# Performance work log

Measured on AMD Instinct MI355X. Metric: run time of the kernel, lower is better.

Reference implementation:

```python
import jax, jax.numpy as jnp
import numpy as np

HIDDEN = 1024
N_HEADS = 16
HEAD_DIM = HIDDEN // N_HEADS
WINDOW = 256
HALF_W = WINDOW // 2  # 128
GLOBAL_TOKENS = (0,)


def setup_inputs() -> dict:
    key = jax.random.key(0)
    ks = jax.random.split(key, 5)
    B, S = 1, 4096
    scale = 0.02
    return {
        "x": jax.random.normal(ks[0], (B, S, HIDDEN), dtype=jnp.float32),
        "Wq": jax.random.normal(ks[1], (HIDDEN, HIDDEN), dtype=jnp.float32) * scale,
        "Wk": jax.random.normal(ks[2], (HIDDEN, HIDDEN), dtype=jnp.float32) * scale,
        "Wv": jax.random.normal(ks[3], (HIDDEN, HIDDEN), dtype=jnp.float32) * scale,
        "Wo": jax.random.normal(ks[4], (HIDDEN, HIDDEN), dtype=jnp.float32) * scale,
    }


def _longformer_mask(seq_len: int) -> jnp.ndarray:
    # sliding window |i-j| <= half_w, plus full rows/cols for global tokens
    idx = jnp.arange(seq_len)
    mask = jnp.abs(idx[:, None] - idx[None, :]) <= HALF_W
    for g in GLOBAL_TOKENS:
        if 0 <= g < seq_len:
            mask = mask.at[g, :].set(True)
            mask = mask.at[:, g].set(True)
    return mask  # [S, S] bool


def reference(x, Wq, Wk, Wv, Wo):
    B, S, H = x.shape
    scale = HEAD_DIM ** -0.5
    # nn.Linear(bias=False): y = x @ W.T ; split heads -> [B, nH, S, hd]
    def proj(W):
        return jnp.einsum('bsh,oh->bso', x, W).reshape(B, S, N_HEADS, HEAD_DIM).transpose(0, 2, 1, 3)
    q, k, v = proj(Wq), proj(Wk), proj(Wv)
    scores = jnp.einsum('bnsd,bntd->bnst', q, k) * scale  # [B, nH, S, S]
    mask = _longformer_mask(S)
    scores = jnp.where(mask[None, None], scores, jnp.float32(-jnp.inf))
    attn = jax.nn.softmax(scores, axis=-1)
    out = jnp.einsum('bnst,bntd->bnsd', attn, v)  # [B, nH, S, hd]
    out = out.transpose(0, 2, 1, 3).reshape(B, S, H)
    return jnp.einsum('bsh,oh->bso', out, Wo)
```

## Files before the change

### kernel.cpp

```cpp
#include <hip/hip_runtime.h>
#include <hip/hip_bf16.h>
#include <stdint.h>

#define S_LEN 4096
#define HID   1024
#define NH    16
#define HD    64
#define HWIN  128

typedef __bf16 bf16x8 __attribute__((ext_vector_type(8)));
typedef float  f32x4  __attribute__((ext_vector_type(4)));
typedef unsigned short u16x8 __attribute__((ext_vector_type(8)));

typedef const __attribute__((address_space(1))) unsigned int* gas_ptr;
typedef __attribute__((address_space(3))) unsigned int* las_ptr;

__device__ __forceinline__ float bf2f(unsigned short u) {
  union { float f; uint32_t i; } w; w.i = ((uint32_t)u) << 16; return w.f;
}
__device__ __forceinline__ unsigned short f2bf(float f) {
  union { float f; uint32_t i; } w; w.f = f;
  uint32_t r = (w.i + 0x7FFFu + ((w.i >> 16) & 1u)) >> 16;
  return (unsigned short)r;
}

__device__ __forceinline__ void gld_lds16(const void* g, void* l) {
  __builtin_amdgcn_global_load_lds((gas_ptr)g, (las_ptr)l, 16, 0, 0);
}

__global__ __launch_bounds__(256) void convert_all(
    const float* __restrict__ x,
    const float* __restrict__ wq, const float* __restrict__ wk,
    const float* __restrict__ wv, const float* __restrict__ wo,
    unsigned short* __restrict__ xb,
    unsigned short* __restrict__ wqb, unsigned short* __restrict__ wkb,
    unsigned short* __restrict__ wvb, unsigned short* __restrict__ wob) {
  const int XF4 = (S_LEN * HID) / 4;
  const int WF4 = (HID * HID) / 4;
  int i = blockIdx.x * 256 + threadIdx.x;
#pragma unroll
  for (int it = 0; it < 4; it++, i += 524288) {
    const float* in; unsigned short* out; int off;
    if (i < XF4) { in = x; out = xb; off = i; }
    else {
      int j = i - XF4;
      int w = j >> 18;
      off = j & (WF4 - 1);
      switch (w) {
        case 0:  in = wq; out = wqb; break;
        case 1:  in = wk; out = wkb; break;
        case 2:  in = wv; out = wvb; break;
        default: in = wo; out = wob; break;
      }
    }
    float4 v = reinterpret_cast<const float4*>(in)[off];
    ushort4 o;
    o.x = f2bf(v.x); o.y = f2bf(v.y); o.z = f2bf(v.z); o.w = f2bf(v.w);
    reinterpret_cast<ushort4*>(out)[off] = o;
  }
}

__device__ __forceinline__ void gemm_body(const unsigned short* __restrict__ A,
                                          const unsigned short* __restrict__ B,
                                          unsigned short* __restrict__ Cb, int mode) {
  __shared__ __align__(16) unsigned short SM[2 * 128 * 64];
  unsigned short* As = SM;
  unsigned short* Bs = SM + 128 * 64;
  constexpr int K = HID;
  const int tid  = threadIdx.x;
  const int lane = tid & 63;
  const int wave = tid >> 6;
  const int wm = wave >> 1, wn = wave & 1;
  const int m0 = blockIdx.x * 128;
  const int n0 = blockIdx.y * 128;
  const int cl = lane & 15, g = lane >> 4;

  f32x4 acc[4][4];
#pragma unroll
  for (int i = 0; i < 4; i++)
#pragma unroll
    for (int j = 0; j < 4; j++) acc[i][j] = f32x4{0.f, 0.f, 0.f, 0.f};

  const unsigned short* Ap[4];
  const unsigned short* Bp[4];
  int ldso[4];
#pragma unroll
  for (int u = 0; u < 4; u++) {
    int s = tid + u * 256;
    int row = s >> 3, c16 = s & 7;
    int sc = ((c16 ^ (row & 7)) << 3);
    Ap[u] = A + (size_t)(m0 + row) * K + sc;
    Bp[u] = B + (size_t)(n0 + row) * K + sc;
    ldso[u] = s * 8;
  }

  for (int k0 = 0; k0 < K; k0 += 64) {
#pragma unroll
    for (int u = 0; u < 4; u++) {
      gld_lds16(Ap[u] + k0, &As[ldso[u]]);
      gld_lds16(Bp[u] + k0, &Bs[ldso[u]]);
    }
    __syncthreads();
#pragma unroll
    for (int kk = 0; kk < 2; kk++) {
      bf16x8 a[4], b[4];
#pragma unroll
      for (int mi = 0; mi < 4; mi++) {
        int row = wm * 64 + mi * 16 + cl;
        int c16 = (kk * 4 + g) ^ (row & 7);
        a[mi] = *reinterpret_cast<const bf16x8*>(&As[row * 64 + c16 * 8]);
      }
#pragma unroll
      for (int ni = 0; ni < 4; ni++) {
        int row = wn * 64 + ni * 16 + cl;
        int c16 = (kk * 4 + g) ^ (row & 7);
        b[ni] = *reinterpret_cast<const bf16x8*>(&Bs[row * 64 + c16 * 8]);
      }
#pragma unroll
      for (int mi = 0; mi < 4; mi++)
#pragma unroll
        for (int ni = 0; ni < 4; ni++)
          acc[mi][ni] = __builtin_amdgcn_mfma_f32_16x16x32_bf16(a[mi], b[ni], acc[mi][ni], 0, 0, 0);
    }
    __syncthreads();
  }

  const int rl = g * 4;
  if (mode == 1) {
#pragma unroll
    for (int mi = 0; mi < 4; mi++)
#pragma unroll
      for (int ni = 0; ni < 4; ni++) {
        int c = wn * 64 + ni * 16 + cl;
        int slot = (wm * 16 + mi * 4 + g) ^ ((c & 7) << 2);
        uint2 u;
        u.x = (uint32_t)f2bf(acc[mi][ni][0]) | ((uint32_t)f2bf(acc[mi][ni][1]) << 16);
        u.y = (uint32_t)f2bf(acc[mi][ni][2]) | ((uint32_t)f2bf(acc[mi][ni][3]) << 16);
        *reinterpret_cast<uint2*>(&SM[c * 128 + slot * 4]) = u;
      }
    __syncthreads();
    const int rgrp = tid & 15;
#pragma unroll
    for (int p = 0; p < 8; p++) {
      int c = p * 16 + (tid >> 4);
      int sa = (2 * rgrp) ^ ((c & 7) << 2);
      int sb = (2 * rgrp + 1) ^ ((c & 7) << 2);
      uint2 a2 = *reinterpret_cast<const uint2*>(&SM[c * 128 + sa * 4]);
      uint2 b2 = *reinterpret_cast<const uint2*>(&SM[c * 128 + sb * 4]);
      uint4 o{a2.x, a2.y, b2.x, b2.y};
      *reinterpret_cast<uint4*>(&Cb[(size_t)(n0 + c) * S_LEN + m0 + rgrp * 8]) = o;
    }
    return;
  }
#pragma unroll
  for (int mi = 0; mi < 4; mi++)
#pragma unroll
    for (int ni = 0; ni < 4; ni++)
#pragma unroll
      for (int i = 0; i < 4; i++) {
        int r = m0 + wm * 64 + mi * 16 + rl + i;
        int c = n0 + wn * 64 + ni * 16 + cl;
        Cb[(size_t)r * HID + c] = f2bf(acc[mi][ni][i]);
      }
}

__global__ __launch_bounds__(256, 2) void gemm_qkv(
    const unsigned short* __restrict__ xb,
    const unsigned short* __restrict__ wqb, const unsigned short* __restrict__ wkb,
    const unsigned short* __restrict__ wvb,
    unsigned short* __restrict__ Qb, unsigned short* __restrict__ Kb,
    unsigned short* __restrict__ Vt) {
  const unsigned short* B = (blockIdx.z == 0) ? wqb : (blockIdx.z == 1) ? wkb : wvb;
  unsigned short* C       = (blockIdx.z == 0) ? Qb  : (blockIdx.z == 1) ? Kb  : Vt;
  int mode = (blockIdx.z == 2) ? 1 : 0;
  gemm_body(xb, B, C, mode);
}

__global__ __launch_bounds__(256, 2) void gemm_proj(
    unsigned short* __restrict__ Ob, const unsigned short* __restrict__ wob,
    const float* __restrict__ mw, const float* __restrict__ lw,
    const float* __restrict__ ow, float* __restrict__ out) {
  if (blockIdx.x == 0) {
    const float LOG2E = 1.44269504f;
    for (int cc = threadIdx.x; cc < HID; cc += 256) {
      int h = cc >> 6, d = cc & 63;
      float m_g = -1e30f;
#pragma unroll
      for (int c = 0; c < 16; c++) m_g = fmaxf(m_g, mw[h * 16 + c]);
      float lsum = 0.f, osum = 0.f;
#pragma unroll
      for (int c = 0; c < 16; c++) {
        float w = exp2f((mw[h * 16 + c] - m_g) * LOG2E);
        lsum += lw[h * 16 + c] * w;
        osum += ow[(size_t)(h * 16 + c) * HD + d] * w;
      }
      Ob[cc] = f2bf(osum / lsum);
    }
    asm volatile("s_waitcnt vmcnt(0)" ::: "memory");
    __syncthreads();
  }

  __shared__ __align__(16) unsigned short As[128 * 64];
  __shared__ __align__(16) unsigned short Bs[64 * 64];
  constexpr int K = HID;
  const int tid  = threadIdx.x;
  const int lane = tid & 63;
  const int wave = tid >> 6;
  const int wm = wave >> 1, wn = wave & 1;
  const int m0 = blockIdx.x * 128;
  const int n0 = blockIdx.y * 64;
  const int cl = lane & 15, g = lane >> 4;

  f32x4 acc[4][2];
#pragma unroll
  for (int i = 0; i < 4; i++)
#pragma unroll
    for (int j = 0; j < 2; j++) acc[i][j] = f32x4{0.f, 0.f, 0.f, 0.f};

  const unsigned short* Ap[4];
  const unsigned short* Bp[2];
  int ldsoA[4], ldsoB[2];
#pragma unroll
  for (int u = 0; u < 4; u++) {
    int s = tid + u * 256;
    int row = s >> 3, c16 = s & 7;
    Ap[u] = Ob + (size_t)(m0 + row) * K + ((c16 ^ (row & 7)) << 3);
    ldsoA[u] = s * 8;
  }
#pragma unroll
  for (int u = 0; u < 2; u++) {
    int s = tid + u * 256;
    int row = s >> 3, c16 = s & 7;
    Bp[u] = wob + (size_t)(n0 + row) * K + ((c16 ^ (row & 7)) << 3);
    ldsoB[u] = s * 8;
  }

  for (int k0 = 0; k0 < K; k0 += 64) {
#pragma unroll
    for (int u = 0; u < 4; u++) gld_lds16(Ap[u] + k0, &As[ldsoA[u]]);
#pragma unroll
    for (int u = 0; u < 2; u++) gld_lds16(Bp[u] + k0, &Bs[ldsoB[u]]);
    __syncthreads();
#pragma unroll
    for (int kk = 0; kk < 2; kk++) {
      bf16x8 a[4], b[2];
#pragma unroll
      for (int mi = 0; mi < 4; mi++) {
        int row = wm * 64 + mi * 16 + cl;
        int c16 = (kk * 4 + g) ^ (row & 7);
        a[mi] = *reinterpret_cast<const bf16x8*>(&As[row * 64 + c16 * 8]);
      }
#pragma unroll
      for (int ni = 0; ni < 2; ni++) {
        int row = wn * 32 + ni * 16 + cl;
        int c16 = (kk * 4 + g) ^ (row & 7);
        b[ni] = *reinterpret_cast<const bf16x8*>(&Bs[row * 64 + c16 * 8]);
      }
#pragma unroll
      for (int mi = 0; mi < 4; mi++)
#pragma unroll
        for (int ni = 0; ni < 2; ni++)
          acc[mi][ni] = __builtin_amdgcn_mfma_f32_16x16x32_bf16(a[mi], b[ni], acc[mi][ni], 0, 0, 0);
    }
    __syncthreads();
  }

  const int rl = g * 4;
#pragma unroll
  for (int mi = 0; mi < 4; mi++)
#pragma unroll
    for (int ni = 0; ni < 2; ni++)
#pragma unroll
      for (int i = 0; i < 4; i++) {
        int r = m0 + wm * 64 + mi * 16 + rl + i;
        int c = n0 + wn * 32 + ni * 16 + cl;
        out[(size_t)r * HID + c] = acc[mi][ni][i];
      }
}

__global__ __launch_bounds__(256) void attn_win(
    const unsigned short* __restrict__ Qb,
    const unsigned short* __restrict__ Kb,
    const unsigned short* __restrict__ Vt,
    unsigned short* __restrict__ Ob,
    float* __restrict__ mw, float* __restrict__ lw, float* __restrict__ ow) {
  const int tid  = threadIdx.x;
  const int lane = tid & 63;
  const int wave = tid >> 6;

  if (blockIdx.x >= 1024) {
    const int bid = blockIdx.x - 1024;
    const int c = bid & 15, h = bid >> 4;
    const int k = c * 256 + tid;
    __shared__ float qsh[HD];
    __shared__ float ps[256];
    __shared__ float redm[4], redl[4];
    __shared__ float red2[4][HD];
    const float LOG2E = 1.44269504f;

    if (tid < HD) qsh[tid] = bf2f(Qb[h * HD + tid]);
    __syncthreads();

    const unsigned short* kr = Kb + (size_t)k * HID + h * HD;
    float acc = 0.f;
#pragma unroll
    for (int v8 = 0; v8 < 8; v8++) {
      u16x8 kv = *reinterpret_cast<const u16x8*>(kr + v8 * 8);
#pragma unroll
      for (int j = 0; j < 8; j++) acc += qsh[v8 * 8 + j] * bf2f(kv[j]);
    }
    float s = acc * 0.125f;

    float m = s;
#pragma unroll
    for (int d = 1; d < 64; d <<= 1) m = fmaxf(m, __shfl_xor(m, d, 64));
    if (lane == 0) redm[wave] = m;
    __syncthreads();
    float m_c = fmaxf(fmaxf(redm[0], redm[1]), fmaxf(redm[2], redm[3]));

    float p = exp2f((s - m_c) * LOG2E);
    ps[tid] = p;
    float l = p;
#pragma unroll
    for (int d = 1; d < 64; d <<= 1) l += __shfl_xor(l, d, 64);
    if (lane == 0) redl[wave] = l;
    __syncthreads();
    float l_c = redl[0] + redl[1] + redl[2] + redl[3];

    const int d = tid & 63, grp = tid >> 6;
    const unsigned short* vrow = Vt + (size_t)(h * HD + d) * S_LEN + c * 256 + grp * 64;
    float a2 = 0.f;
#pragma unroll
    for (int v8 = 0; v8 < 8; v8++) {
      u16x8 vv = *reinterpret_cast<const u16x8*>(vrow + v8 * 8);
#pragma unroll
      for (int j = 0; j < 8; j++) a2 += ps[grp * 64 + v8 * 8 + j] * bf2f(vv[j]);
    }
    red2[grp][d] = a2;
    __syncthreads();
    if (tid < HD) {
      float o = red2[0][tid] + red2[1][tid] + red2[2][tid] + red2[3][tid];
      ow[(size_t)(h * 16 + c) * HD + tid] = o;
    }
    if (tid == 0) { mw[h * 16 + c] = m_c; lw[h * 16 + c] = l_c; }
    return;
  }

  __shared__ __align__(16) unsigned short Kl[2][64 * 64];
  __shared__ __align__(16) unsigned short Vl[2][64 * 64];
  __shared__ __align__(16) unsigned short Ps[4][16 * 64];
  const int L  = (blockIdx.x & 7) * 128 + (blockIdx.x >> 3);
  const int h  = L >> 6;
  const int q0 = (L & 63) * 64;
  const int qr   = q0 + wave * 16;
  const int cl = lane & 15, g = lane >> 4, rl = g * 4;
  const float SCL = 0.125f * 1.44269504f;

  int kw0 = q0 - 128; if (kw0 < 0) kw0 = 0;
  int kw1 = q0 + 192; if (kw1 > S_LEN) kw1 = S_LEN;
  const int nc = (kw1 - kw0) >> 6;

  const int s0 = tid, s1 = tid + 256;
  const int kr0 = s0 >> 3, kc0 = ((s0 & 7) ^ (kr0 & 7)) << 3;
  const int kr1 = s1 >> 3, kc1 = ((s1 & 7) ^ (kr1 & 7)) << 3;
  const unsigned short* Kbase = Kb + h * HD;
  const unsigned short* Vbase = Vt + (size_t)h * HD * S_LEN;

  auto stage = [&](int kb, int b) {
    gld_lds16(Kbase + (size_t)(kb + kr0) * HID + kc0, &Kl[b][s0 * 8]);
    gld_lds16(Kbase + (size_t)(kb + kr1) * HID + kc1, &Kl[b][s1 * 8]);
    gld_lds16(Vbase + (size_t)kr0 * S_LEN + kb + kc0, &Vl[b][s0 * 8]);
    gld_lds16(Vbase + (size_t)kr1 * S_LEN + kb + kc1, &Vl[b][s1 * 8]);
  };

  stage(kw0, 0);

  bf16x8 qf[2], k0f[2];
  {
    const unsigned short* qb = Qb + (size_t)(qr + cl) * HID + h * HD + g * 8;
    qf[0] = *reinterpret_cast<const bf16x8*>(qb);
    qf[1] = *reinterpret_cast<const bf16x8*>(qb + 32);
    const unsigned short* k0 = Kb + h * HD + g * 8;
    k0f[0] = *reinterpret_cast<const bf16x8*>(k0);
    k0f[1] = *reinterpret_cast<const bf16x8*>(k0 + 32);
  }
  float v0[4];
#pragma unroll
  for (int nt = 0; nt < 4; nt++)
    v0[nt] = bf2f(Vt[(size_t)(h * HD + nt * 16 + cl) * S_LEN]);

  float m_i[4] = {-1e30f, -1e30f, -1e30f, -1e30f};
  float l_i[4] = {0.f, 0.f, 0.f, 0.f};
  f32x4 oacc[4];
#pragma unroll
  for (int nt = 0; nt < 4; nt++) oacc[nt] = f32x4{0.f, 0.f, 0.f, 0.f};

  __syncthreads();

  for (int c = 0; c < nc; c++) {
    const int cur = c & 1;
    const int kb = kw0 + c * 64;
    if (c + 1 < nc) stage(kw0 + (c + 1) * 64, cur ^ 1);

    bf16x8 kf[4][2];
#pragma unroll
    for (int t = 0; t < 4; t++) {
      int R = t * 16 + cl;
      kf[t][0] = *reinterpret_cast<const bf16x8*>(&Kl[cur][R * 64 + ((g ^ (R & 7)) << 3)]);
      kf[t][1] = *reinterpret_cast<const bf16x8*>(&Kl[cur][R * 64 + (((g + 4) ^ (R & 7)) << 3)]);
    }
    f32x4 s4[4];
    __builtin_amdgcn_s_setprio(1);
#pragma unroll
    for (int t = 0; t < 4; t++) {
      s4[t] = f32x4{0.f, 0.f, 0.f, 0.f};
      s4[t] = __builtin_amdgcn_mfma_f32_16x16x32_bf16(qf[0], kf[t][0], s4[t], 0, 0, 0);
      s4[t] = __builtin_amdgcn_mfma_f32_16x16x32_bf16(qf[1], kf[t][1], s4[t], 0, 0, 0);
    }
    __builtin_amdgcn_s_setprio(0);

    float sv[4][4], tm[4];
    if (kb >= qr - 113 && kb <= qr + 65) {
#pragma unroll
      for (int i = 0; i < 4; i++) {
        tm[i] = -1e30f;
#pragma unroll
        for (int t = 0; t < 4; t++) {
          float v = s4[t][i] * SCL;
          sv[t][i] = v;
          tm[i] = fmaxf(tm[i], v);
        }
      }
    } else {
#pragma unroll
      for (int i = 0; i < 4; i++) {
        int row = qr + rl + i;
        tm[i] = -1e30f;
#pragma unroll
        for (int t = 0; t < 4; t++) {
          int col = kb + t * 16 + cl;
          int d = row - col;
          float v = (d <= HWIN && d >= -HWIN) ? s4[t][i] * SCL : -1e30f;
          sv[t][i] = v;
          tm[i] = fmaxf(tm[i], v);
        }
      }
    }
#pragma unroll
    for (int dd = 1; dd < 16; dd <<= 1)
#pragma unroll
      for (int i = 0; i < 4; i++) tm[i] = fmaxf(tm[i], __shfl_xor(tm[i], dd, 16));

    float p[4][4], ps[4];
#pragma unroll
    for (int i = 0; i < 4; i++) {
      float mnew = fmaxf(m_i[i], tm[i]);
      float fac  = exp2f(m_i[i] - mnew);
      m_i[i] = mnew;
      float sum = 0.f;
#pragma unroll
      for (int t = 0; t < 4; t++) { p[t][i] = exp2f(sv[t][i] - mnew); sum += p[t][i]; }
      ps[i] = sum;
      l_i[i] *= fac;
#pragma unroll
      for (int nt = 0; nt < 4; nt++) oacc[nt][i] *= fac;
    }
#pragma unroll
    for (int dd = 1; dd < 16; dd <<= 1)
#pragma unroll
      for (int i = 0; i < 4; i++) ps[i] += __shfl_xor(ps[i], dd, 16);
#pragma unroll
    for (int i = 0; i < 4; i++) l_i[i] += ps[i];

#pragma unroll
    for (int t = 0; t < 4; t++)
#pragma unroll
      for (int i = 0; i < 4; i++) {
        int row = rl + i;
        Ps[wave][row * 64 + ((t * 16 + cl) ^ ((row & 7) << 3))] = f2bf(p[t][i]);
      }
    bf16x8 pf[2];
    pf[0] = *reinterpret_cast<const bf16x8*>(&Ps[wave][cl * 64 + ((g * 8) ^ ((cl & 7) << 3))]);
    pf[1] = *reinterpret_cast<const bf16x8*>(&Ps[wave][cl * 64 + ((32 + g * 8) ^ ((cl & 7) << 3))]);

    __builtin_amdgcn_s_setprio(1);
#pragma unroll
    for (int nt = 0; nt < 4; nt++) {
      int row = nt * 16 + cl;
      bf16x8 vf0 = *reinterpret_cast<const bf16x8*>(&Vl[cur][row * 64 + ((g ^ (row & 7)) << 3)]);
      bf16x8 vf1 = *reinterpret_cast<const bf16x8*>(&Vl[cur][row * 64 + (((g + 4) ^ (row & 7)) << 3)]);
      oacc[nt] = __builtin_amdgcn_mfma_f32_16x16x32_bf16(pf[0], vf0, oacc[nt], 0, 0, 0);
      oacc[nt] = __builtin_amdgcn_mfma_f32_16x16x32_bf16(pf[1], vf1, oacc[nt], 0, 0, 0);
    }
    __builtin_amdgcn_s_setprio(0);

    __syncthreads();
  }

  float part = 0.f;
#pragma unroll
  for (int s = 0; s < 2; s++)
#pragma unroll
    for (int j = 0; j < 8; j++) part += (float)qf[s][j] * (float)k0f[s][j];
  part += __shfl_xor(part, 16);
  part += __shfl_xor(part, 32);
  float s0q = part * SCL;
#pragma unroll
  for (int i = 0; i < 4; i++) {
    float z0 = __shfl(s0q, rl + i, 16);
    int row = qr + rl + i;
    if (row > HWIN) {
      float mnew = fmaxf(m_i[i], z0);
      float fac  = exp2f(m_i[i] - mnew);
      float p0   = exp2f(z0 - mnew);
      l_i[i] = l_i[i] * fac + p0;
#pragma unroll
      for (int nt = 0; nt < 4; nt++)
        oacc[nt][i] = oacc[nt][i] * fac + p0 * v0[nt];
    }
  }

#pragma unroll
  for (int nt = 0; nt < 4; nt++)
#pragma unroll
    for (int i = 0; i < 4; i++)
      Ob[(size_t)(qr + rl + i) * HID + h * HD + nt * 16 + cl] = f2bf(oacc[nt][i] / l_i[i]);
}

extern "C" void kernel_launch(void* const* d_in, const int* in_sizes, int n_in,
                              void* d_out, int out_size, void* d_ws, size_t ws_size,
                              hipStream_t stream) {
  const float* x  = (const float*)d_in[0];
  const float* wq = (const float*)d_in[1];
  const float* wk = (const float*)d_in[2];
  const float* wv = (const float*)d_in[3];
  const float* wo = (const float*)d_in[4];
  float* out = (float*)d_out;
  char* ws = (char*)d_ws;
  const size_t MB = 1024ull * 1024ull;
  unsigned short* xb  = (unsigned short*)(ws + 0 * MB);
  unsigned short* wqb = (unsigned short*)(ws + 8 * MB);
  unsigned short* wkb = (unsigned short*)(ws + 10 * MB);
  unsigned short* wvb = (unsigned short*)(ws + 12 * MB);
  unsigned short* wob = (unsigned short*)(ws + 14 * MB);
  unsigned short* Qb  = (unsigned short*)(ws + 16 * MB);
  unsigned short* Kb  = (unsigned short*)(ws + 24 * MB);
  unsigned short* Vt  = (unsigned short*)(ws + 32 * MB);
  unsigned short* Ob  = (unsigned short*)(ws + 40 * MB);
  float* mw = (float*)(ws + 48 * MB);
  float* lw = (float*)(ws + 48 * MB + 4096);
  float* ow = (float*)(ws + 48 * MB + 8192);

  dim3 blk(256);
  convert_all<<<dim3(2048), blk, 0, stream>>>(
      x, wq, wk, wv, wo, xb, wqb, wkb, wvb, wob);
  gemm_qkv<<<dim3(S_LEN / 128, HID / 128, 3), blk, 0, stream>>>(
      xb, wqb, wkb, wvb, Qb, Kb, Vt);
  attn_win<<<dim3(1280), blk, 0, stream>>>(Qb, Kb, Vt, Ob, mw, lw, ow);
  gemm_proj<<<dim3(S_LEN / 128, HID / 64), blk, 0, stream>>>(
      Ob, wob, mw, lw, ow, out);
}
```

Baseline: 89.15 us.

## Narrow QKV GEMM tile to 128x64 and skip softmax rescale when max stable

```diff
diff --git a/kernel.cpp b/kernel.cpp
--- a/kernel.cpp
+++ b/kernel.cpp
@@ -60,50 +60,60 @@
   }
 }
 
-__device__ __forceinline__ void gemm_body(const unsigned short* __restrict__ A,
-                                          const unsigned short* __restrict__ B,
-                                          unsigned short* __restrict__ Cb, int mode) {
-  __shared__ __align__(16) unsigned short SM[2 * 128 * 64];
+__global__ __launch_bounds__(256, 2) void gemm_qkv(
+    const unsigned short* __restrict__ xb,
+    const unsigned short* __restrict__ wqb, const unsigned short* __restrict__ wkb,
+    const unsigned short* __restrict__ wvb,
+    unsigned short* __restrict__ Qb, unsigned short* __restrict__ Kb,
+    unsigned short* __restrict__ Vt) {
+  __shared__ __align__(16) unsigned short SM[128 * 64 + 64 * 64];
   unsigned short* As = SM;
   unsigned short* Bs = SM + 128 * 64;
+  const unsigned short* B = (blockIdx.z == 0) ? wqb : (blockIdx.z == 1) ? wkb : wvb;
+  unsigned short* Cb      = (blockIdx.z == 0) ? Qb  : (blockIdx.z == 1) ? Kb  : Vt;
+  const int mode = (blockIdx.z == 2) ? 1 : 0;
   constexpr int K = HID;
   const int tid  = threadIdx.x;
   const int lane = tid & 63;
   const int wave = tid >> 6;
   const int wm = wave >> 1, wn = wave & 1;
   const int m0 = blockIdx.x * 128;
-  const int n0 = blockIdx.y * 128;
+  const int n0 = blockIdx.y * 64;
   const int cl = lane & 15, g = lane >> 4;
 
-  f32x4 acc[4][4];
+  f32x4 acc[4][2];
 #pragma unroll
   for (int i = 0; i < 4; i++)
 #pragma unroll
-    for (int j = 0; j < 4; j++) acc[i][j] = f32x4{0.f, 0.f, 0.f, 0.f};
+    for (int j = 0; j < 2; j++) acc[i][j] = f32x4{0.f, 0.f, 0.f, 0.f};
 
   const unsigned short* Ap[4];
-  const unsigned short* Bp[4];
-  int ldso[4];
+  const unsigned short* Bp[2];
+  int ldsoA[4], ldsoB[2];
 #pragma unroll
   for (int u = 0; u < 4; u++) {
     int s = tid + u * 256;
     int row = s >> 3, c16 = s & 7;
-    int sc = ((c16 ^ (row & 7)) << 3);
-    Ap[u] = A + (size_t)(m0 + row) * K + sc;
-    Bp[u] = B + (size_t)(n0 + row) * K + sc;
-    ldso[u] = s * 8;
+    Ap[u] = xb + (size_t)(m0 + row) * K + ((c16 ^ (row & 7)) << 3);
+    ldsoA[u] = s * 8;
+  }
+#pragma unroll
+  for (int u = 0; u < 2; u++) {
+    int s = tid + u * 256;
+    int row = s >> 3, c16 = s & 7;
+    Bp[u] = B + (size_t)(n0 + row) * K + ((c16 ^ (row & 7)) << 3);
+    ldsoB[u] = s * 8;
   }
 
   for (int k0 = 0; k0 < K; k0 += 64) {
 #pragma unroll
-    for (int u = 0; u < 4; u++) {
-      gld_lds16(Ap[u] + k0, &As[ldso[u]]);
-      gld_lds16(Bp[u] + k0, &Bs[ldso[u]]);
-    }
+    for (int u = 0; u < 4; u++) gld_lds16(Ap[u] + k0, &As[ldsoA[u]]);
+#pragma unroll
+    for (int u = 0; u < 2; u++) gld_lds16(Bp[u] + k0, &Bs[ldsoB[u]]);
     __syncthreads();
 #pragma unroll
     for (int kk = 0; kk < 2; kk++) {
-      bf16x8 a[4], b[4];
+      bf16x8 a[4], b[2];
 #pragma unroll
       for (int mi = 0; mi < 4; mi++) {
         int row = wm * 64 + mi * 16 + cl;
@@ -111,15 +121,15 @@
         a[mi] = *reinterpret_cast<const bf16x8*>(&As[row * 64 + c16 * 8]);
       }
 #pragma unroll
-      for (int ni = 0; ni < 4; ni++) {
-        int row = wn * 64 + ni * 16 + cl;
+      for (int ni = 0; ni < 2; ni++) {
+        int row = wn * 32 + ni * 16 + cl;
         int c16 = (kk * 4 + g) ^ (row & 7);
         b[ni] = *reinterpret_cast<const bf16x8*>(&Bs[row * 64 + c16 * 8]);
       }
 #pragma unroll
       for (int mi = 0; mi < 4; mi++)
 #pragma unroll
-        for (int ni = 0; ni < 4; ni++)
+        for (int ni = 0; ni < 2; ni++)
           acc[mi][ni] = __builtin_amdgcn_mfma_f32_16x16x32_bf16(a[mi], b[ni], acc[mi][ni], 0, 0, 0);
     }
     __syncthreads();
@@ -130,8 +140,8 @@
 #pragma unroll
     for (int mi = 0; mi < 4; mi++)
 #pragma unroll
-      for (int ni = 0; ni < 4; ni++) {
-        int c = wn * 64 + ni * 16 + cl;
+      for (int ni = 0; ni < 2; ni++) {
+        int c = wn * 32 + ni * 16 + cl;
         int slot = (wm * 16 + mi * 4 + g) ^ ((c & 7) << 2);
         uint2 u;
         u.x = (uint32_t)f2bf(acc[mi][ni][0]) | ((uint32_t)f2bf(acc[mi][ni][1]) << 16);
@@ -141,7 +151,7 @@
     __syncthreads();
     const int rgrp = tid & 15;
 #pragma unroll
-    for (int p = 0; p < 8; p++) {
+    for (int p = 0; p < 4; p++) {
       int c = p * 16 + (tid >> 4);
       int sa = (2 * rgrp) ^ ((c & 7) << 2);
       int sb = (2 * rgrp + 1) ^ ((c & 7) << 2);
@@ -155,25 +165,13 @@
 #pragma unroll
   for (int mi = 0; mi < 4; mi++)
 #pragma unroll
-    for (int ni = 0; ni < 4; ni++)
+    for (int ni = 0; ni < 2; ni++)
 #pragma unroll
       for (int i = 0; i < 4; i++) {
         int r = m0 + wm * 64 + mi * 16 + rl + i;
-        int c = n0 + wn * 64 + ni * 16 + cl;
+        int c = n0 + wn * 32 + ni * 16 + cl;
         Cb[(size_t)r * HID + c] = f2bf(acc[mi][ni][i]);
       }
-}
-
-__global__ __launch_bounds__(256, 2) void gemm_qkv(
-    const unsigned short* __restrict__ xb,
-    const unsigned short* __restrict__ wqb, const unsigned short* __restrict__ wkb,
-    const unsigned short* __restrict__ wvb,
-    unsigned short* __restrict__ Qb, unsigned short* __restrict__ Kb,
-    unsigned short* __restrict__ Vt) {
-  const unsigned short* B = (blockIdx.z == 0) ? wqb : (blockIdx.z == 1) ? wkb : wvb;
-  unsigned short* C       = (blockIdx.z == 0) ? Qb  : (blockIdx.z == 1) ? Kb  : Vt;
-  int mode = (blockIdx.z == 2) ? 1 : 0;
-  gemm_body(xb, B, C, mode);
 }
 
 __global__ __launch_bounds__(256, 2) void gemm_proj(
@@ -446,24 +444,37 @@
         }
       }
     }
-#pragma unroll
-    for (int dd = 1; dd < 16; dd <<= 1)
-#pragma unroll
-      for (int i = 0; i < 4; i++) tm[i] = fmaxf(tm[i], __shfl_xor(tm[i], dd, 16));
-
+
+    bool ok = true;
+#pragma unroll
+    for (int i = 0; i < 4; i++) ok = ok && (tm[i] <= m_i[i] + 8.0f);
     float p[4][4], ps[4];
-#pragma unroll
-    for (int i = 0; i < 4; i++) {
-      float mnew = fmaxf(m_i[i], tm[i]);
-      float fac  = exp2f(m_i[i] - mnew);
-      m_i[i] = mnew;
-      float sum = 0.f;
-#pragma unroll
-      for (int t = 0; t < 4; t++) { p[t][i] = exp2f(sv[t][i] - mnew); sum += p[t][i]; }
-      ps[i] = sum;
-      l_i[i] *= fac;
-#pragma unroll
-      for (int nt = 0; nt < 4; nt++) oacc[nt][i] *= fac;
+    if (__all((int)ok)) {
+#pragma unroll
+      for (int i = 0; i < 4; i++) {
+        float sum = 0.f;
+#pragma unroll
+        for (int t = 0; t < 4; t++) { p[t][i] = exp2f(sv[t][i] - m_i[i]); sum += p[t][i]; }
+        ps[i] = sum;
+      }
+    } else {
+#pragma unroll
+      for (int dd = 1; dd < 16; dd <<= 1)
+#pragma unroll
+        for (int i = 0; i < 4; i++) tm[i] = fmaxf(tm[i], __shfl_xor(tm[i], dd, 16));
+#pragma unroll
+      for (int i = 0; i < 4; i++) {
+        float mnew = fmaxf(m_i[i], tm[i]);
+        float fac  = exp2f(m_i[i] - mnew);
+        m_i[i] = mnew;
+        float sum = 0.f;
+#pragma unroll
+        for (int t = 0; t < 4; t++) { p[t][i] = exp2f(sv[t][i] - mnew); sum += p[t][i]; }
+        ps[i] = sum;
+        l_i[i] *= fac;
+#pragma unroll
+        for (int nt = 0; nt < 4; nt++) oacc[nt][i] *= fac;
+      }
     }
 #pragma unroll
     for (int dd = 1; dd < 16; dd <<= 1)
@@ -554,7 +565,7 @@
   dim3 blk(256);
   convert_all<<<dim3(2048), blk, 0, stream>>>(
       x, wq, wk, wv, wo, xb, wqb, wkb, wvb, wob);
-  gemm_qkv<<<dim3(S_LEN / 128, HID / 128, 3), blk, 0, stream>>>(
+  gemm_qkv<<<dim3(S_LEN / 128, HID / 64, 3), blk, 0, stream>>>(
       xb, wqb, wkb, wvb, Qb, Kb, Vt);
   attn_win<<<dim3(1280), blk, 0, stream>>>(Qb, Kb, Vt, Ob, mw, lw, ow);
   gemm_proj<<<dim3(S_LEN / 128, HID / 64), blk, 0, stream>>>(
```

Result: slower. 93.26 us (+4.6%).
